# Performance work log

Measured on AMD Instinct MI355X. Metric: run time of the kernel, lower is better.

Reference implementation:

```python
import jax, jax.numpy as jnp
import numpy as np

N_QUBITS = 3
N_LAYERS = 3


def _ry(theta):
    # theta: scalar or (B,) -> (2,2) or (B,2,2) real rotation cast to complex
    h = theta * 0.5
    c, s = jnp.cos(h), jnp.sin(h)
    return jnp.stack([jnp.stack([c, -s], -1), jnp.stack([s, c], -1)], -2).astype(jnp.complex64)


def _rz(theta):
    # diag(e^{-i t/2}, e^{+i t/2})
    e = jnp.exp(-0.5j * theta.astype(jnp.complex64))
    z = jnp.zeros_like(e)
    return jnp.stack([jnp.stack([e, z], -1), jnp.stack([z, jnp.conj(e)], -1)], -2)


def _apply_gate(state, U, q):
    # state: (B,2,2,2) with axes (batch,q0,q1,q2); U: (2,2) shared or (B,2,2) per-sample
    axes = 'xyz'
    a = axes[q]
    pre = 'b' if U.ndim == 3 else ''
    return jnp.einsum(f'{pre}i{a},b{axes}->b{axes.replace(a, "i")}', U, state)


def _cnot01(s):  # control q0 (axis1), target q1 (axis2)
    return jnp.concatenate([s[:, :1], s[:, 1:, ::-1]], axis=1)


def _cnot12(s):  # control q1 (axis2), target q2 (axis3)
    return jnp.concatenate([s[:, :, :1], s[:, :, 1:][..., ::-1]], axis=2)


def _vqc(inputs, q_weights):
    B = inputs.shape[0]
    # |000> for every sample
    state = jnp.zeros((B, 8), jnp.complex64).at[:, 0].set(1.0).reshape(B, 2, 2, 2)
    # angle encoding: RY(inputs[i]) on wire i (i % 8 == i for i in 0..2)
    for q in range(N_QUBITS):
        state = _apply_gate(state, _ry(inputs[:, q]), q)
    for l in range(N_LAYERS):
        for q in range(N_QUBITS):
            state = _apply_gate(state, _ry(q_weights[l, q, 0]), q)
            state = _apply_gate(state, _rz(q_weights[l, q, 1]), q)
        state = _cnot01(state)
        state = _cnot12(state)
    # <Z_0> = P(q0=0) - P(q0=1)
    probs = jnp.square(jnp.abs(state.reshape(B, 2, 4)))
    z = probs[:, 0].sum(-1) - probs[:, 1].sum(-1)
    return z[:, None].astype(jnp.float32)  # (B,1) like tf.expand_dims


def setup_inputs() -> dict:
    key = jax.random.key(0)
    k1, k2 = jax.random.split(key)
    B = 1048576
    inputs = jax.random.normal(k1, (B, 8), dtype=jnp.float32)
    q_weights = jax.random.normal(k2, (N_LAYERS, N_QUBITS, 2), dtype=jnp.float32) * 0.05
    return {"inputs": inputs, "q_weights": q_weights}


def reference(inputs, q_weights):
    return _vqc(inputs, q_weights)
```

## Files before the change

### kernel.cpp

```cpp
#include <hip/hip_runtime.h>

__global__ __launch_bounds__(64) void vqc_coeffs_kernel(
    const float* __restrict__ w, float* __restrict__ Bout) {
    const int lane = threadIdx.x;
    const int i = lane >> 3;

    float vr = (i == (lane & 7)) ? 1.f : 0.f;
    float vi = 0.f;

#pragma unroll
    for (int l = 0; l < 3; ++l) {
#pragma unroll
        for (int q = 0; q < 3; ++q) {
            const int m = 4 >> q;
            const int d = m << 3;
            {
                float th = 0.5f * w[(l * 3 + q) * 2 + 0];
                float s, c;
                __sincosf(th, &s, &c);
                float pr = __shfl_xor(vr, d, 64);
                float pi = __shfl_xor(vi, d, 64);
                float t = (i & m) ? s : -s;
                vr = c * vr + t * pr;
                vi = c * vi + t * pi;
            }
            {
                float ph = 0.5f * w[(l * 3 + q) * 2 + 1];
                float sz, cz;
                __sincosf(ph, &sz, &cz);
                float ei = (i & m) ? sz : -sz;
                float nr = cz * vr - ei * vi;
                float ni = cz * vi + ei * vr;
                vr = nr; vi = ni;
            }
        }
        {
            float pr = __shfl_xor(vr, 16, 64);
            float pi = __shfl_xor(vi, 16, 64);
            if (i & 4) { vr = pr; vi = pi; }
        }
        {
            float pr = __shfl_xor(vr, 8, 64);
            float pi = __shfl_xor(vi, 8, 64);
            if (i & 2) { vr = pr; vi = pi; }
        }
    }

    __shared__ float LUr[64], LUi[64], LM[64];
    LUr[lane] = vr; LUi[lane] = vi;
    __syncthreads();

    {
        const int jj = lane >> 3, kk = lane & 7;
        float acc = 0.f;
#pragma unroll
        for (int ii = 0; ii < 8; ++ii) {
            float t = LUr[ii * 8 + jj] * LUr[ii * 8 + kk] +
                      LUi[ii * 8 + jj] * LUi[ii * 8 + kk];
            acc += (ii < 4) ? t : -t;
        }
        LM[lane] = acc;
    }
    __syncthreads();

    if (lane == 0) {
        float M[8][8];
#pragma unroll
        for (int a = 0; a < 8; ++a)
#pragma unroll
            for (int b = 0; b < 8; ++b) M[a][b] = LM[a * 8 + b];

        float T1[3][4][4];
#pragma unroll
        for (int jl = 0; jl < 4; ++jl)
#pragma unroll
            for (int kl = 0; kl < 4; ++kl) {
                T1[0][jl][kl] = 0.5f * (M[jl][kl] + M[4 + jl][4 + kl]);
                T1[1][jl][kl] = 0.5f * (M[jl][kl] - M[4 + jl][4 + kl]);
                T1[2][jl][kl] = 0.5f * (M[jl][4 + kl] + M[4 + jl][kl]);
            }
        float T2[3][3][2][2];
#pragma unroll
        for (int a = 0; a < 3; ++a)
#pragma unroll
            for (int c = 0; c < 2; ++c)
#pragma unroll
                for (int cp = 0; cp < 2; ++cp) {
                    T2[a][0][c][cp] = 0.5f * (T1[a][c][cp] + T1[a][2 + c][2 + cp]);
                    T2[a][1][c][cp] = 0.5f * (T1[a][c][cp] - T1[a][2 + c][2 + cp]);
                    T2[a][2][c][cp] = 0.5f * (T1[a][c][2 + cp] + T1[a][2 + c][cp]);
                }
#pragma unroll
        for (int a = 0; a < 3; ++a)
#pragma unroll
            for (int b = 0; b < 3; ++b) {
                Bout[(a * 3 + b) * 3 + 0] = 0.5f * (T2[a][b][0][0] + T2[a][b][1][1]);
                Bout[(a * 3 + b) * 3 + 1] = 0.5f * (T2[a][b][0][0] - T2[a][b][1][1]);
                Bout[(a * 3 + b) * 3 + 2] = 0.5f * (T2[a][b][0][1] + T2[a][b][1][0]);
            }
        Bout[27] = 0.f;
    }
}

__global__ __launch_bounds__(256) void vqc_eval_kernel(
    const float* __restrict__ in, const float* __restrict__ coeffs,
    float* __restrict__ out, int B) {
    __shared__ float Bs[28];
    const int t = threadIdx.x;
    if (t < 7) reinterpret_cast<float4*>(Bs)[t] =
        reinterpret_cast<const float4*>(coeffs)[t];
    __syncthreads();

    const int b = blockIdx.x * 256 + t;
    if (b >= B) return;

    const float4 v = reinterpret_cast<const float4*>(in)[2 * b];
    float s0, c0, s1, c1, s2, c2;
    __sincosf(v.x, &s0, &c0);
    __sincosf(v.y, &s1, &c1);
    __sincosf(v.z, &s2, &c2);

    float e0 = 0.f, e1 = 0.f, e2 = 0.f;
#pragma unroll
    for (int a = 0; a < 3; ++a) {
        float h0 = Bs[(a * 3 + 0) * 3 + 0] + Bs[(a * 3 + 0) * 3 + 1] * c2 + Bs[(a * 3 + 0) * 3 + 2] * s2;
        float h1 = Bs[(a * 3 + 1) * 3 + 0] + Bs[(a * 3 + 1) * 3 + 1] * c2 + Bs[(a * 3 + 1) * 3 + 2] * s2;
        float h2 = Bs[(a * 3 + 2) * 3 + 0] + Bs[(a * 3 + 2) * 3 + 1] * c2 + Bs[(a * 3 + 2) * 3 + 2] * s2;
        float ea = h0 + h1 * c1 + h2 * s1;
        if (a == 0) e0 = ea; else if (a == 1) e1 = ea; else e2 = ea;
    }
    out[b] = e0 + e1 * c0 + e2 * s0;
}

extern "C" void kernel_launch(void* const* d_in, const int* in_sizes, int n_in,
                              void* d_out, int out_size, void* d_ws, size_t ws_size,
                              hipStream_t stream) {
    const float* inputs = (const float*)d_in[0];
    const float* qw     = (const float*)d_in[1];
    float* out          = (float*)d_out;
    float* coeffs       = (float*)d_ws;

    const int B = in_sizes[0] / 8;

    vqc_coeffs_kernel<<<1, 64, 0, stream>>>(qw, coeffs);
    const int blocks = (B + 255) / 256;
    vqc_eval_kernel<<<blocks, 256, 0, stream>>>(inputs, coeffs, out, B);
}
```

Baseline: 75.86 us.

## Fuse coefficient computation into eval kernel and process four samples per thread

Merges the single-block coefficient kernel into the evaluation kernel, so every block recomputes the 8x8 unitary and the 27 coefficients redundantly in shared memory. This removes one kernel launch and the serial dependency between the two launches. Each thread now handles four samples and issues their input loads before the coefficient computation, so the memory latency overlaps with the redundant math. The cost is per-block duplicated work, including a serial single-thread stage and extra barriers.

```diff
diff --git a/kernel.cpp b/kernel.cpp
--- a/kernel.cpp
+++ b/kernel.cpp
@@ -1,69 +1,82 @@
 #include <hip/hip_runtime.h>
 
-__global__ __launch_bounds__(64) void vqc_coeffs_kernel(
-    const float* __restrict__ w, float* __restrict__ Bout) {
-    const int lane = threadIdx.x;
-    const int i = lane >> 3;
+__global__ __launch_bounds__(256) void vqc_fused_kernel(
+    const float* __restrict__ in, const float* __restrict__ w,
+    float* __restrict__ out, int B) {
+    __shared__ float LUr[64], LUi[64], LM[64];
+    __shared__ float Bs[27];
 
-    float vr = (i == (lane & 7)) ? 1.f : 0.f;
-    float vi = 0.f;
+    const int t = threadIdx.x;
+    const int base = blockIdx.x * 1024 + t;
+
+    float4 v[4];
+#pragma unroll
+    for (int k = 0; k < 4; ++k) {
+        const int b = base + k * 256;
+        if (b < B) v[k] = reinterpret_cast<const float4*>(in)[2 * b];
+    }
+
+    if (t < 64) {
+        const int lane = t;
+        const int i = lane >> 3;
+        float vr = (i == (lane & 7)) ? 1.f : 0.f;
+        float vi = 0.f;
 
 #pragma unroll
-    for (int l = 0; l < 3; ++l) {
+        for (int l = 0; l < 3; ++l) {
 #pragma unroll
-        for (int q = 0; q < 3; ++q) {
-            const int m = 4 >> q;
-            const int d = m << 3;
-            {
-                float th = 0.5f * w[(l * 3 + q) * 2 + 0];
-                float s, c;
-                __sincosf(th, &s, &c);
-                float pr = __shfl_xor(vr, d, 64);
-                float pi = __shfl_xor(vi, d, 64);
-                float t = (i & m) ? s : -s;
-                vr = c * vr + t * pr;
-                vi = c * vi + t * pi;
+            for (int q = 0; q < 3; ++q) {
+                const int m = 4 >> q;
+                const int d = m << 3;
+                {
+                    float th = 0.5f * w[(l * 3 + q) * 2 + 0];
+                    float s, c;
+                    __sincosf(th, &s, &c);
+                    float pr = __shfl_xor(vr, d, 64);
+                    float pi = __shfl_xor(vi, d, 64);
+                    float sgn = (i & m) ? s : -s;
+                    vr = c * vr + sgn * pr;
+                    vi = c * vi + sgn * pi;
+                }
+                {
+                    float ph = 0.5f * w[(l * 3 + q) * 2 + 1];
+                    float sz, cz;
+                    __sincosf(ph, &sz, &cz);
+                    float ei = (i & m) ? sz : -sz;
+                    float nr = cz * vr - ei * vi;
+                    float ni = cz * vi + ei * vr;
+                    vr = nr; vi = ni;
+                }
             }
             {
-                float ph = 0.5f * w[(l * 3 + q) * 2 + 1];
-                float sz, cz;
-                __sincosf(ph, &sz, &cz);
-                float ei = (i & m) ? sz : -sz;
-                float nr = cz * vr - ei * vi;
-                float ni = cz * vi + ei * vr;
-                vr = nr; vi = ni;
+                float pr = __shfl_xor(vr, 16, 64);
+                float pi = __shfl_xor(vi, 16, 64);
+                if (i & 4) { vr = pr; vi = pi; }
+            }
+            {
+                float pr = __shfl_xor(vr, 8, 64);
+                float pi = __shfl_xor(vi, 8, 64);
+                if (i & 2) { vr = pr; vi = pi; }
             }
         }
-        {
-            float pr = __shfl_xor(vr, 16, 64);
-            float pi = __shfl_xor(vi, 16, 64);
-            if (i & 4) { vr = pr; vi = pi; }
-        }
-        {
-            float pr = __shfl_xor(vr, 8, 64);
-            float pi = __shfl_xor(vi, 8, 64);
-            if (i & 2) { vr = pr; vi = pi; }
-        }
+        LUr[lane] = vr; LUi[lane] = vi;
     }
-
-    __shared__ float LUr[64], LUi[64], LM[64];
-    LUr[lane] = vr; LUi[lane] = vi;
     __syncthreads();
 
-    {
-        const int jj = lane >> 3, kk = lane & 7;
+    if (t < 64) {
+        const int jj = t >> 3, kk = t & 7;
         float acc = 0.f;
 #pragma unroll
         for (int ii = 0; ii < 8; ++ii) {
-            float t = LUr[ii * 8 + jj] * LUr[ii * 8 + kk] +
+            float s = LUr[ii * 8 + jj] * LUr[ii * 8 + kk] +
                       LUi[ii * 8 + jj] * LUi[ii * 8 + kk];
-            acc += (ii < 4) ? t : -t;
+            acc += (ii < 4) ? s : -s;
         }
-        LM[lane] = acc;
+        LM[t] = acc;
     }
     __syncthreads();
 
-    if (lane == 0) {
+    if (t == 0) {
         float M[8][8];
 #pragma unroll
         for (int a = 0; a < 8; ++a)
@@ -94,42 +107,33 @@
         for (int a = 0; a < 3; ++a)
 #pragma unroll
             for (int b = 0; b < 3; ++b) {
-                Bout[(a * 3 + b) * 3 + 0] = 0.5f * (T2[a][b][0][0] + T2[a][b][1][1]);
-                Bout[(a * 3 + b) * 3 + 1] = 0.5f * (T2[a][b][0][0] - T2[a][b][1][1]);
-                Bout[(a * 3 + b) * 3 + 2] = 0.5f * (T2[a][b][0][1] + T2[a][b][1][0]);
+                Bs[(a * 3 + b) * 3 + 0] = 0.5f * (T2[a][b][0][0] + T2[a][b][1][1]);
+                Bs[(a * 3 + b) * 3 + 1] = 0.5f * (T2[a][b][0][0] - T2[a][b][1][1]);
+                Bs[(a * 3 + b) * 3 + 2] = 0.5f * (T2[a][b][0][1] + T2[a][b][1][0]);
             }
-        Bout[27] = 0.f;
     }
-}
-
-__global__ __launch_bounds__(256) void vqc_eval_kernel(
-    const float* __restrict__ in, const float* __restrict__ coeffs,
-    float* __restrict__ out, int B) {
-    __shared__ float Bs[28];
-    const int t = threadIdx.x;
-    if (t < 7) reinterpret_cast<float4*>(Bs)[t] =
-        reinterpret_cast<const float4*>(coeffs)[t];
     __syncthreads();
 
-    const int b = blockIdx.x * 256 + t;
-    if (b >= B) return;
+#pragma unroll
+    for (int k = 0; k < 4; ++k) {
+        const int b = base + k * 256;
+        if (b >= B) continue;
+        float s0, c0, s1, c1, s2, c2;
+        __sincosf(v[k].x, &s0, &c0);
+        __sincosf(v[k].y, &s1, &c1);
+        __sincosf(v[k].z, &s2, &c2);
 
-    const float4 v = reinterpret_cast<const float4*>(in)[2 * b];
-    float s0, c0, s1, c1, s2, c2;
-    __sincosf(v.x, &s0, &c0);
-    __sincosf(v.y, &s1, &c1);
-    __sincosf(v.z, &s2, &c2);
-
-    float e0 = 0.f, e1 = 0.f, e2 = 0.f;
+        float e0 = 0.f, e1 = 0.f, e2 = 0.f;
 #pragma unroll
-    for (int a = 0; a < 3; ++a) {
-        float h0 = Bs[(a * 3 + 0) * 3 + 0] + Bs[(a * 3 + 0) * 3 + 1] * c2 + Bs[(a * 3 + 0) * 3 + 2] * s2;
-        float h1 = Bs[(a * 3 + 1) * 3 + 0] + Bs[(a * 3 + 1) * 3 + 1] * c2 + Bs[(a * 3 + 1) * 3 + 2] * s2;
-        float h2 = Bs[(a * 3 + 2) * 3 + 0] + Bs[(a * 3 + 2) * 3 + 1] * c2 + Bs[(a * 3 + 2) * 3 + 2] * s2;
-        float ea = h0 + h1 * c1 + h2 * s1;
-        if (a == 0) e0 = ea; else if (a == 1) e1 = ea; else e2 = ea;
+        for (int a = 0; a < 3; ++a) {
+            float h0 = Bs[(a * 3 + 0) * 3 + 0] + Bs[(a * 3 + 0) * 3 + 1] * c2 + Bs[(a * 3 + 0) * 3 + 2] * s2;
+            float h1 = Bs[(a * 3 + 1) * 3 + 0] + Bs[(a * 3 + 1) * 3 + 1] * c2 + Bs[(a * 3 + 1) * 3 + 2] * s2;
+            float h2 = Bs[(a * 3 + 2) * 3 + 0] + Bs[(a * 3 + 2) * 3 + 1] * c2 + Bs[(a * 3 + 2) * 3 + 2] * s2;
+            float ea = h0 + h1 * c1 + h2 * s1;
+            if (a == 0) e0 = ea; else if (a == 1) e1 = ea; else e2 = ea;
+        }
+        out[b] = e0 + e1 * c0 + e2 * s0;
     }
-    out[b] = e0 + e1 * c0 + e2 * s0;
 }
 
 extern "C" void kernel_launch(void* const* d_in, const int* in_sizes, int n_in,
@@ -138,11 +142,8 @@
     const float* inputs = (const float*)d_in[0];
     const float* qw     = (const float*)d_in[1];
     float* out          = (float*)d_out;
-    float* coeffs       = (float*)d_ws;
 
     const int B = in_sizes[0] / 8;
-
-    vqc_coeffs_kernel<<<1, 64, 0, stream>>>(qw, coeffs);
-    const int blocks = (B + 255) / 256;
-    vqc_eval_kernel<<<blocks, 256, 0, stream>>>(inputs, coeffs, out, B);
+    const int blocks = (B + 1023) / 1024;
+    vqc_fused_kernel<<<blocks, 256, 0, stream>>>(inputs, qw, out, B);
 }
```

New measurement: 76.01 us. About the same (+0.2%).
